# Kernel optimization log

Measured on AMD Instinct MI355X. Metric: run time of the kernel, lower is better.

Reference implementation:

```python
import jax, jax.numpy as jnp
import numpy as np

B, S, H, E, K = 4, 4096, 2048, 64, 2
LN_EPS = 1e-5
AUX_EPS = 1e-9


def setup_inputs() -> dict:
    key = jax.random.key(0)
    ks = jax.random.split(key, 5)
    lim1 = 1.0 / np.sqrt(H)
    x = jax.random.normal(ks[0], (B, S, H), dtype=jnp.float32)
    W1 = jax.random.uniform(ks[1], (H, H), jnp.float32, -lim1, lim1)
    b1 = jax.random.uniform(ks[2], (H,), jnp.float32, -lim1, lim1)
    W2 = jax.random.uniform(ks[3], (H, E), jnp.float32, -lim1, lim1)
    b2 = jax.random.uniform(ks[4], (E,), jnp.float32, -lim1, lim1)
    gamma = jnp.ones((H,), jnp.float32)
    beta = jnp.zeros((H,), jnp.float32)
    return {"x": x, "W1": W1, "b1": b1, "W2": W2, "b2": b2, "gamma": gamma, "beta": beta}


def reference(x, W1, b1, W2, b2, gamma, beta):
    # LayerNorm over hidden dim
    mu = jnp.mean(x, axis=-1, keepdims=True)
    var = jnp.mean(jnp.square(x - mu), axis=-1, keepdims=True)
    x_norm = (x - mu) * jax.lax.rsqrt(var + LN_EPS) * gamma + beta
    # 2-layer router MLP: Linear -> ReLU -> Linear
    h = jax.nn.relu(jnp.einsum('bsh,hk->bsk', x_norm, W1) + b1)
    logits = jnp.einsum('bsh,he->bse', h, W2) + b2  # [B,S,E]
    probs = jax.nn.softmax(logits, axis=-1)
    # top-k + renormalize
    top_k_probs, top_k_indices = jax.lax.top_k(probs, K)
    top_k_probs = top_k_probs / jnp.sum(top_k_probs, axis=-1, keepdims=True)
    # aux load-balancing loss
    p_expert = jnp.mean(probs, axis=(0, 1))  # [E]
    aux_loss = jnp.sum(p_expert * jnp.log(p_expert * E + AUX_EPS))
    return top_k_indices, top_k_probs, aux_loss
```

## Files before the change

### kernel.cpp

```cpp
#include <hip/hip_runtime.h>
#include <hip/hip_fp16.h>
#include <cstdint>
#include <cstddef>

#define HH   2048
#define MM   16384
#define NE   64
#define FIXCAP 3072
#define MARGIN 1.0e-3f
#define LN_EPS  1e-5f
#define AUX_EPS 1e-9f

typedef __attribute__((ext_vector_type(8))) _Float16 f16x8;
typedef __attribute__((ext_vector_type(4))) _Float16 f16x4;
typedef __attribute__((ext_vector_type(4))) float    f32x4;

__device__ __forceinline__ void gload_lds16(const void* g, void* l) {
    __builtin_amdgcn_global_load_lds(
        (const __attribute__((address_space(1))) unsigned int*)g,
        (__attribute__((address_space(3))) unsigned int*)l,
        16, 0, 0);
}

__device__ __forceinline__ uint32_t swz64(uint32_t x) {
    return x ^ (((x >> 7) & 3u) << 4) ^ (((x >> 9) & 1u) << 6);
}
__device__ __forceinline__ uint32_t swz128(uint32_t x) {
    return x ^ (((x >> 8) & 7u) << 4);
}

__global__ __launch_bounds__(256) void k_tw1(const float* __restrict__ W1,
                                             _Float16* __restrict__ whp,
                                             _Float16* __restrict__ wlp) {
    __shared__ float tile[32][33];
    int tx = threadIdx.x & 31;
    int ty = threadIdx.x >> 5;
    int bx = blockIdx.x & 63;
    int by = blockIdx.x >> 6;
#pragma unroll
    for (int i = 0; i < 4; ++i) {
        int k = by * 32 + ty + i * 8;
        tile[ty + i * 8][tx] = W1[(size_t)k * HH + bx * 32 + tx];
    }
    __syncthreads();
#pragma unroll
    for (int i = 0; i < 4; ++i) {
        int n = bx * 32 + ty + i * 8;
        float w = tile[tx][ty + i * 8];
        _Float16 hi = (_Float16)w;
        _Float16 lo = (_Float16)((w - (float)hi) * 1024.0f);
        whp[(size_t)n * HH + by * 32 + tx] = hi;
        wlp[(size_t)n * HH + by * 32 + tx] = lo;
    }
}

__global__ __launch_bounds__(256) void k_w2q(const float* __restrict__ W2,
                                             _Float16* __restrict__ w2q) {
    int e = blockIdx.x;
    int t = threadIdx.x;
#pragma unroll
    for (int j = 0; j < 8; ++j) {
        int c = t * 8 + j;
        float w = W2[(size_t)c * NE + e];
        _Float16 hi = (_Float16)w;
        _Float16 lo = (_Float16)((w - (float)hi) * 1024.0f);
        f16x4 q = {hi, hi, lo, (_Float16)0.0f};
        *(f16x4*)&w2q[(size_t)e * 8192 + (size_t)c * 4] = q;
    }
}

__global__ __launch_bounds__(256) void k_ln(const float* __restrict__ x,
                                            const float* __restrict__ gamma,
                                            const float* __restrict__ beta,
                                            _Float16* __restrict__ xh,
                                            _Float16* __restrict__ xl) {
    int row = blockIdx.x * 4 + (threadIdx.x >> 6);
    int lane = threadIdx.x & 63;
    const float4* xr = (const float4*)(x + (size_t)row * HH);
    float4 v[8];
    float s = 0.f, sq = 0.f;
#pragma unroll
    for (int j = 0; j < 8; ++j) {
        v[j] = xr[lane + j * 64];
        s  += v[j].x + v[j].y + v[j].z + v[j].w;
        sq += v[j].x*v[j].x + v[j].y*v[j].y + v[j].z*v[j].z + v[j].w*v[j].w;
    }
#pragma unroll
    for (int m = 1; m < 64; m <<= 1) { s += __shfl_xor(s, m); sq += __shfl_xor(sq, m); }
    float mu  = s * (1.0f / HH);
    float var = sq * (1.0f / HH) - mu * mu;
    float rr  = rsqrtf(var + LN_EPS);

    const float4* gr = (const float4*)gamma;
    const float4* br = (const float4*)beta;
#pragma unroll
    for (int j = 0; j < 8; ++j) {
        int idx = lane + j * 64;
        float4 g = gr[idx];
        float4 b = br[idx];
        float f[4];
        f[0] = (v[j].x - mu) * rr * g.x + b.x;
        f[1] = (v[j].y - mu) * rr * g.y + b.y;
        f[2] = (v[j].z - mu) * rr * g.z + b.z;
        f[3] = (v[j].w - mu) * rr * g.w + b.w;
        f16x4 oh, ol;
#pragma unroll
        for (int q = 0; q < 4; ++q) {
            _Float16 hi = (_Float16)f[q];
            oh[q] = hi;
            ol[q] = (_Float16)(f[q] - (float)hi);
        }
        *(f16x4*)&xh[(size_t)row * HH + idx * 4] = oh;
        *(f16x4*)&xl[(size_t)row * HH + idx * 4] = ol;
    }
}

#define VMW(N) do { asm volatile("s_waitcnt vmcnt(" #N ")" ::: "memory"); \
                    __builtin_amdgcn_sched_barrier(0); } while (0)

#define STAGE1(KT) do { uint32_t kb = (uint32_t)(KT) * 64;                     \
    char* dst = lds + (((KT) & 3) << 15);                                      \
    gload_lds16(pxh + gA0 + kb, dst + dstb0);                                  \
    gload_lds16(pxh + gA1 + kb, dst + dstb1);                                  \
    gload_lds16(pwh + gB0 + kb, dst + 16384 + dstb0);                          \
    gload_lds16(pwh + gB1 + kb, dst + 16384 + dstb1);                          \
} while (0)

__global__ __launch_bounds__(512, 2) void k_gemm1(const _Float16* __restrict__ Ah_g,
                                                  const _Float16* __restrict__ Bh_g,
                                                  const _Float16* __restrict__ w2q,
                                                  const float* __restrict__ b1,
                                                  float* __restrict__ part) {
    __shared__ __align__(16) char lds[131072];

    int xcd = blockIdx.x & 7;
    int idx = blockIdx.x >> 3;
    int bm  = xcd * 8 + (idx >> 3);
    int bn  = idx & 7;
    int t = threadIdx.x;
    int lane = t & 63;
    int wid = t >> 6;
    int wm = wid >> 2;
    int wn = wid & 3;
    int r16 = lane & 15, ko = lane >> 4;

    f32x4 acc[8][4];
#pragma unroll
    for (int m = 0; m < 8; ++m)
#pragma unroll
        for (int n = 0; n < 4; ++n)
            acc[m][n] = (f32x4){0.f, 0.f, 0.f, 0.f};

    const char* pxh = (const char*)Ah_g;
    const char* pwh = (const char*)Bh_g;

    uint32_t dstb0 = (uint32_t)t * 16;
    uint32_t dstb1 = 8192 + dstb0;
    uint32_t L0 = swz64(dstb0), L1 = swz64(dstb1);
    uint32_t gA0 = ((uint32_t)bm * 256 + (L0 >> 6)) * (HH * 2) + (L0 & 63);
    uint32_t gA1 = ((uint32_t)bm * 256 + (L1 >> 6)) * (HH * 2) + (L1 & 63);
    uint32_t gB0 = ((uint32_t)bn * 256 + (L0 >> 6)) * (HH * 2) + (L0 & 63);
    uint32_t gB1 = ((uint32_t)bn * 256 + (L1 >> 6)) * (HH * 2) + (L1 & 63);

    uint32_t aoff[8], boff[4];
#pragma unroll
    for (int m = 0; m < 8; ++m)
        aoff[m] = swz64((uint32_t)(wm * 128 + m * 16 + r16) * 64 + ko * 16);
#pragma unroll
    for (int n = 0; n < 4; ++n)
        boff[n] = swz64((uint32_t)(wn * 64 + n * 16 + r16) * 64 + ko * 16);

    STAGE1(0);
    STAGE1(1);
    STAGE1(2);
    VMW(8);
    __builtin_amdgcn_s_barrier();

    for (int kt = 0; kt < 64; ++kt) {
        char* slot = lds + ((kt & 3) << 15);
        const char* Axh = slot;
        const char* Bwh = slot + 16384;

        f16x8 fbh[4], fah[4];
#pragma unroll
        for (int n = 0; n < 4; ++n) fbh[n] = *(const f16x8*)(Bwh + boff[n]);
#pragma unroll
        for (int m = 0; m < 4; ++m) fah[m] = *(const f16x8*)(Axh + aoff[m]);
        if (kt < 61) STAGE1(kt + 3);
        __builtin_amdgcn_s_setprio(1);
#pragma unroll
        for (int m = 0; m < 4; ++m)
#pragma unroll
            for (int n = 0; n < 4; ++n)
                acc[m][n] = __builtin_amdgcn_mfma_f32_16x16x32_f16(fah[m], fbh[n], acc[m][n], 0, 0, 0);
        __builtin_amdgcn_s_setprio(0);
#pragma unroll
        for (int m = 0; m < 4; ++m) fah[m] = *(const f16x8*)(Axh + aoff[4 + m]);
        __builtin_amdgcn_s_setprio(1);
#pragma unroll
        for (int m = 0; m < 4; ++m)
#pragma unroll
            for (int n = 0; n < 4; ++n)
                acc[4 + m][n] = __builtin_amdgcn_mfma_f32_16x16x32_f16(fah[m], fbh[n], acc[4 + m][n], 0, 0, 0);
        __builtin_amdgcn_s_setprio(0);
        if (kt < 61)      VMW(8);
        else if (kt == 61) VMW(4);
        else if (kt == 62) VMW(0);
        __builtin_amdgcn_s_barrier();
    }

    char* A2 = lds;
    char* B2 = lds + 32768;

    float bv[4];
#pragma unroll
    for (int n = 0; n < 4; ++n)
        bv[n] = b1[bn * 256 + wn * 64 + n * 16 + r16];

    f32x4 acc2[2][4];
#pragma unroll
    for (int mf = 0; mf < 2; ++mf)
#pragma unroll
        for (int ef = 0; ef < 4; ++ef)
            acc2[mf][ef] = (f32x4){0.f, 0.f, 0.f, 0.f};

    int hi4 = lane >> 4;
    int ko16 = ko * 16;

#pragma unroll
    for (int c = 0; c < 16; ++c) {
        {
            int e = t >> 3;
            int cb = (t & 7) * 16;
            const char* src = (const char*)w2q + (size_t)e * 16384
                            + (size_t)bn * 2048 + (size_t)c * 128 + cb;
            *(f16x8*)(B2 + swz128((uint32_t)e * 128 + cb)) = *(const f16x8*)src;
        }
        if (wn == (c >> 2)) {
            const int n = c & 3;
#pragma unroll
            for (int m = 0; m < 8; ++m)
#pragma unroll
                for (int i = 0; i < 4; ++i) {
                    float h = acc[m][n][i] + bv[n];
                    h = fmaxf(h, 0.f);
                    _Float16 hh = (_Float16)h;
                    float hhf = (float)hh;
                    _Float16 hl = (_Float16)(h - hhf);
                    _Float16 hs = (_Float16)(hhf * 0.0009765625f);
                    int row = wm * 128 + m * 16 + hi4 * 4 + i;
                    f16x4 q = {hh, hl, hs, (_Float16)0.0f};
                    *(f16x4*)(A2 + swz128((uint32_t)row * 128 + r16 * 8)) = q;
                }
        }
        __syncthreads();
#pragma unroll
        for (int kk = 0; kk < 2; ++kk) {
            f16x8 bfr[4];
#pragma unroll
            for (int ef = 0; ef < 4; ++ef)
                bfr[ef] = *(const f16x8*)(B2 +
                    swz128((uint32_t)(ef * 16 + r16) * 128 + kk * 64 + ko16));
#pragma unroll
            for (int mf = 0; mf < 2; ++mf) {
                f16x8 afr = *(const f16x8*)(A2 +
                    swz128((uint32_t)(wid * 32 + mf * 16 + r16) * 128 + kk * 64 + ko16));
#pragma unroll
                for (int ef = 0; ef < 4; ++ef)
                    acc2[mf][ef] = __builtin_amdgcn_mfma_f32_16x16x32_f16(
                        afr, bfr[ef], acc2[mf][ef], 0, 0, 0);
            }
        }
        __syncthreads();
    }

#pragma unroll
    for (int mf = 0; mf < 2; ++mf)
#pragma unroll
        for (int i = 0; i < 4; ++i) {
            int grow = bm * 256 + wid * 32 + mf * 16 + hi4 * 4 + i;
            float* dst = part + ((size_t)bn * MM + grow) * NE;
#pragma unroll
            for (int ef = 0; ef < 4; ++ef)
                dst[ef * 16 + r16] = acc2[mf][ef][i];
        }
}

__global__ __launch_bounds__(64) void k_screen(const float* __restrict__ part,
                                               const float* __restrict__ b2,
                                               float* __restrict__ out,
                                               float* __restrict__ sums,
                                               int* __restrict__ list,
                                               int* __restrict__ cnt) {
    int lane = threadIdx.x;
    int r = blockIdx.x * 64 + lane;
    float l[NE];
#pragma unroll
    for (int e = 0; e < NE; e += 4) {
        float4 b = *(const float4*)&b2[e];
        l[e] = b.x; l[e + 1] = b.y; l[e + 2] = b.z; l[e + 3] = b.w;
    }
    for (int sl = 0; sl < 8; ++sl) {
        const float* ps = part + ((size_t)sl * MM + r) * NE;
#pragma unroll
        for (int e = 0; e < NE; e += 4) {
            float4 v = *(const float4*)&ps[e];
            l[e] += v.x; l[e + 1] += v.y; l[e + 2] += v.z; l[e + 3] += v.w;
        }
    }
    float m1 = -1e30f, m2 = -1e30f, m3 = -1e30f;
    int i1 = 0, i2 = 0;
#pragma unroll
    for (int e = 0; e < NE; ++e) {
        if (l[e] > m1)      { m3 = m2; m2 = m1; i2 = i1; m1 = l[e]; i1 = e; }
        else if (l[e] > m2) { m3 = m2; m2 = l[e]; i2 = e; }
        else if (l[e] > m3) { m3 = l[e]; }
    }
    float ev[NE];
    float Z = 0.f;
#pragma unroll
    for (int e = 0; e < NE; ++e) { ev[e] = expf(l[e] - m1); Z += ev[e]; }

    float eb = expf(m2 - m1);
    float pa = 1.0f / (1.0f + eb);
    float pb = eb * pa;

    out[(size_t)r * 2 + 0] = (float)i1;
    out[(size_t)r * 2 + 1] = (float)i2;
    out[(size_t)2 * MM + r * 2 + 0] = pa;
    out[(size_t)2 * MM + r * 2 + 1] = pb;

    if ((m1 - m2 < MARGIN) || (m2 - m3 < MARGIN)) {
        int s = atomicAdd(cnt, 1);
        if (s < FIXCAP) list[s] = r;
    }

    float invZ = 1.0f / Z;
    float keep = 0.f;
#pragma unroll
    for (int e = 0; e < NE; ++e) {
        float q = ev[e] * invZ;
#pragma unroll
        for (int sh = 1; sh < 64; sh <<= 1) q += __shfl_xor(q, sh);
        if (lane == e) keep = q;
    }
    atomicAdd(&sums[lane], keep);
}

#define VMW0 do { asm volatile("s_waitcnt vmcnt(0)" ::: "memory"); \
                  __builtin_amdgcn_sched_barrier(0); } while (0)

#define STAGEF_A(KT) do { uint32_t kb = (uint32_t)(KT) * 64;                   \
    char* dst = lds + (((KT) & 1) << 16);                                      \
    gload_lds16(pxh + gA0 + kb, dst + dstb0);                                  \
    gload_lds16(pxh + gA1 + kb, dst + dstb1);                                  \
    gload_lds16(pxl + gA0 + kb, dst + 16384 + dstb0);                          \
    gload_lds16(pxl + gA1 + kb, dst + 16384 + dstb1);                          \
} while (0)

#define STAGEF_B(KT) do { uint32_t kb = (uint32_t)(KT) * 64;                   \
    char* dst = lds + (((KT) & 1) << 16) + 32768;                              \
    gload_lds16(pwh + gB0 + kb, dst + dstb0);                                  \
    gload_lds16(pwh + gB1 + kb, dst + dstb1);                                  \
    gload_lds16(pwl + gB0 + kb, dst + 16384 + dstb0);                          \
    gload_lds16(pwl + gB1 + kb, dst + 16384 + dstb1);                          \
} while (0)

__global__ __launch_bounds__(512, 2) void k_fixg(const _Float16* __restrict__ Ah_g,
                                                 const _Float16* __restrict__ Al_g,
                                                 const _Float16* __restrict__ Bh_g,
                                                 const _Float16* __restrict__ Bl_g,
                                                 const int* __restrict__ list,
                                                 const int* __restrict__ cnt,
                                                 float* __restrict__ hpart) {
    int ks = blockIdx.x & 3;
    int bn = (blockIdx.x >> 2) & 7;
    int bm = blockIdx.x >> 5;
    int cv = *cnt; if (cv > FIXCAP) cv = FIXCAP;
    if (bm * 256 >= cv) return;

    __shared__ __align__(16) char lds[131072];
    int t = threadIdx.x;
    int lane = t & 63;
    int wid = t >> 6;
    int wm = wid >> 2;
    int wn = wid & 3;
    int r16 = lane & 15, ko = lane >> 4;

    f32x4 acc[8][4];
#pragma unroll
    for (int m = 0; m < 8; ++m)
#pragma unroll
        for (int n = 0; n < 4; ++n)
            acc[m][n] = (f32x4){0.f, 0.f, 0.f, 0.f};

    const char* pxh = (const char*)Ah_g;
    const char* pxl = (const char*)Al_g;
    const char* pwh = (const char*)Bh_g;
    const char* pwl = (const char*)Bl_g;

    uint32_t dstb0 = (uint32_t)t * 16;
    uint32_t dstb1 = 8192 + dstb0;
    uint32_t L0 = swz64(dstb0), L1 = swz64(dstb1);
    int rA0 = list[bm * 256 + (L0 >> 6)];
    int rA1 = list[bm * 256 + (L1 >> 6)];
    uint32_t kso = (uint32_t)ks * 1024;
    uint32_t gA0 = (uint32_t)rA0 * (HH * 2) + (L0 & 63) + kso;
    uint32_t gA1 = (uint32_t)rA1 * (HH * 2) + (L1 & 63) + kso;
    uint32_t gB0 = ((uint32_t)bn * 256 + (L0 >> 6)) * (HH * 2) + (L0 & 63) + kso;
    uint32_t gB1 = ((uint32_t)bn * 256 + (L1 >> 6)) * (HH * 2) + (L1 & 63) + kso;

    uint32_t aoff[8], boff[4];
#pragma unroll
    for (int m = 0; m < 8; ++m)
        aoff[m] = swz64((uint32_t)(wm * 128 + m * 16 + r16) * 64 + ko * 16);
#pragma unroll
    for (int n = 0; n < 4; ++n)
        boff[n] = swz64((uint32_t)(wn * 64 + n * 16 + r16) * 64 + ko * 16);

    STAGEF_A(0);
    STAGEF_B(0);
    VMW0;
    __builtin_amdgcn_s_barrier();

    for (int kt = 0; kt < 16; ++kt) {
        char* slot = lds + ((kt & 1) << 16);
        const char* Axh = slot;
        const char* Axl = slot + 16384;
        const char* Bwh = slot + 32768;
        const char* Bwl = slot + 49152;

        f16x8 fbh[4], fbl[4], fah[4], fal[4];
#pragma unroll
        for (int n = 0; n < 4; ++n) {
            fbh[n] = *(const f16x8*)(Bwh + boff[n]);
            fbl[n] = *(const f16x8*)(Bwl + boff[n]);
        }
#pragma unroll
        for (int m = 0; m < 4; ++m) {
            fah[m] = *(const f16x8*)(Axh + aoff[m]);
            fal[m] = *(const f16x8*)(Axl + aoff[m]);
        }
        if (kt < 15) STAGEF_A(kt + 1);
        __builtin_amdgcn_s_setprio(1);
#pragma unroll
        for (int m = 0; m < 4; ++m) {
            f16x8 fas = fah[m] * (_Float16)0.0009765625f;
#pragma unroll
            for (int n = 0; n < 4; ++n) {
                acc[m][n] = __builtin_amdgcn_mfma_f32_16x16x32_f16(fah[m], fbh[n], acc[m][n], 0, 0, 0);
                acc[m][n] = __builtin_amdgcn_mfma_f32_16x16x32_f16(fal[m], fbh[n], acc[m][n], 0, 0, 0);
                acc[m][n] = __builtin_amdgcn_mfma_f32_16x16x32_f16(fas,    fbl[n], acc[m][n], 0, 0, 0);
            }
        }
        __builtin_amdgcn_s_setprio(0);

#pragma unroll
        for (int m = 0; m < 4; ++m) {
            fah[m] = *(const f16x8*)(Axh + aoff[4 + m]);
            fal[m] = *(const f16x8*)(Axl + aoff[4 + m]);
        }
        if (kt < 15) STAGEF_B(kt + 1);
        __builtin_amdgcn_s_setprio(1);
#pragma unroll
        for (int m = 0; m < 4; ++m) {
            f16x8 fas = fah[m] * (_Float16)0.0009765625f;
#pragma unroll
            for (int n = 0; n < 4; ++n) {
                acc[4 + m][n] = __builtin_amdgcn_mfma_f32_16x16x32_f16(fah[m], fbh[n], acc[4 + m][n], 0, 0, 0);
                acc[4 + m][n] = __builtin_amdgcn_mfma_f32_16x16x32_f16(fal[m], fbh[n], acc[4 + m][n], 0, 0, 0);
                acc[4 + m][n] = __builtin_amdgcn_mfma_f32_16x16x32_f16(fas,    fbl[n], acc[4 + m][n], 0, 0, 0);
            }
        }
        __builtin_amdgcn_s_setprio(0);
        if (kt < 15) VMW0;
        __builtin_amdgcn_s_barrier();
    }

    float* hp = hpart + (size_t)ks * FIXCAP * HH;
    int hi4 = lane >> 4;
#pragma unroll
    for (int m = 0; m < 8; ++m)
#pragma unroll
        for (int n = 0; n < 4; ++n)
#pragma unroll
            for (int i = 0; i < 4; ++i) {
                int row_l = bm * 256 + wm * 128 + m * 16 + hi4 * 4 + i;
                int col = bn * 256 + wn * 64 + n * 16 + r16;
                hp[(size_t)row_l * HH + col] = acc[m][n][i];
            }
}

__global__ __launch_bounds__(256) void k_fix2(const float* __restrict__ hpart,
                                              const float* __restrict__ b1,
                                              const float* __restrict__ W2,
                                              const float* __restrict__ b2,
                                              const int* __restrict__ list,
                                              const int* __restrict__ cnt,
                                              float* __restrict__ out) {
    int n = *cnt; if (n > FIXCAP) n = FIXCAP;
    int gi = blockIdx.x;
    if (gi >= n) return;
    int r = list[gi];
    int e = threadIdx.x & 63;
    int kg = threadIdx.x >> 6;
    const float* h0 = hpart + (size_t)gi * HH;
    const float* h1 = h0 + (size_t)FIXCAP * HH;
    const float* h2 = h1 + (size_t)FIXCAP * HH;
    const float* h3 = h2 + (size_t)FIXCAP * HH;
    float p = 0.f;
    int k0 = kg * 512;
    for (int k = k0; k < k0 + 512; ++k) {
        float h = ((h0[k] + h1[k]) + (h2[k] + h3[k])) + b1[k];
        h = fmaxf(h, 0.f);
        p = fmaf(h, W2[(size_t)k * NE + e], p);
    }
    __shared__ float red[4][NE];
    red[kg][e] = p;
    __syncthreads();
    if (threadIdx.x < 64) {
        float l = ((red[0][e] + red[1][e]) + (red[2][e] + red[3][e])) + b2[e];
        float m1 = l;
#pragma unroll
        for (int sh = 1; sh < 64; sh <<= 1) m1 = fmaxf(m1, __shfl_xor(m1, sh));
        unsigned long long bb = __ballot(l == m1);
        int i1 = (int)(__ffsll((long long)bb) - 1);
        float l2 = (e == i1) ? -1e30f : l;
        float m2 = l2;
#pragma unroll
        for (int sh = 1; sh < 64; sh <<= 1) m2 = fmaxf(m2, __shfl_xor(m2, sh));
        unsigned long long bb2 = __ballot(l2 == m2);
        int i2 = (int)(__ffsll((long long)bb2) - 1);
        if (e == 0) {
            float eb = expf(m2 - m1);
            float pa = 1.0f / (1.0f + eb);
            float pb = eb * pa;
            out[(size_t)r * 2 + 0] = (float)i1;
            out[(size_t)r * 2 + 1] = (float)i2;
            out[(size_t)2 * MM + r * 2 + 0] = pa;
            out[(size_t)2 * MM + r * 2 + 1] = pb;
        }
    }
}

__global__ void k_aux(const float* __restrict__ sums, float* __restrict__ out) {
    if (threadIdx.x == 0) {
        float loss = 0.f;
        for (int e = 0; e < NE; ++e) {
            float p = sums[e] * (1.0f / MM);
            loss += p * logf(p * (float)NE + AUX_EPS);
        }
        out[(size_t)4 * MM] = loss;
    }
}

extern "C" void kernel_launch(void* const* d_in, const int* in_sizes, int n_in,
                              void* d_out, int out_size, void* d_ws, size_t ws_size,
                              hipStream_t stream) {
    const float* x     = (const float*)d_in[0];
    const float* W1    = (const float*)d_in[1];
    const float* b1    = (const float*)d_in[2];
    const float* W2    = (const float*)d_in[3];
    const float* b2    = (const float*)d_in[4];
    const float* gamma = (const float*)d_in[5];
    const float* beta  = (const float*)d_in[6];
    float* out = (float*)d_out;

    char* ws = (char*)d_ws;
    _Float16* xh   = (_Float16*)(ws);
    _Float16* xl   = (_Float16*)(ws + 67108864);
    _Float16* whp  = (_Float16*)(ws + 134217728);
    _Float16* wlp  = (_Float16*)(ws + 142606336);
    _Float16* w2q  = (_Float16*)(ws + 150994944);
    float*    part = (float*)   (ws + 152043520);
    float*   hpart = (float*)   (ws + 152043520);
    int*      list = (int*)     (ws + 252706816);
    float*    sums = (float*)   (ws + 252719104);
    int*      cnt  = (int*)     (ws + 252719360);

    hipMemsetAsync(sums, 0, 512, stream);
    hipMemsetAsync(list, 0, FIXCAP * 4, stream);
    k_tw1   <<<4096,    256, 0, stream>>>(W1, whp, wlp);
    k_w2q   <<<64,      256, 0, stream>>>(W2, w2q);
    k_ln    <<<MM/4,    256, 0, stream>>>(x, gamma, beta, xh, xl);
    k_gemm1 <<<512,     512, 0, stream>>>(xh, whp, w2q, b1, part);
    k_screen<<<MM/64,   64,  0, stream>>>(part, b2, out, sums, list, cnt);
    k_fixg  <<<384,     512, 0, stream>>>(xh, xl, whp, wlp, list, cnt, hpart);
    k_fix2  <<<FIXCAP,  256, 0, stream>>>(hpart, b1, W2, b2, list, cnt, out);
    k_aux   <<<1,       64,  0, stream>>>(sums, out);
}
```

Measured before the change: 368.5 us.

## Compute low-half LN residual only for flagged rows and fuse small kernels

The full LayerNorm pass now writes only the fp16 high part, which removes the 64 MB xl write. A new kernel recomputes LayerNorm hi/lo for just the flagged rows into compact gathered buffers. k_fixg then reads those contiguously instead of gathering through the list. The W1/W2 prep kernels are merged into one launch, the aux-loss kernel is folded into k_fix2, and the two memsets become one, cutting launch count.

```diff
diff --git a/kernel.cpp b/kernel.cpp
--- a/kernel.cpp
+++ b/kernel.cpp
@@ -29,9 +29,25 @@
     return x ^ (((x >> 8) & 7u) << 4);
 }
 
-__global__ __launch_bounds__(256) void k_tw1(const float* __restrict__ W1,
-                                             _Float16* __restrict__ whp,
-                                             _Float16* __restrict__ wlp) {
+__global__ __launch_bounds__(256) void k_prep(const float* __restrict__ W1,
+                                              const float* __restrict__ W2,
+                                              _Float16* __restrict__ whp,
+                                              _Float16* __restrict__ wlp,
+                                              _Float16* __restrict__ w2q) {
+    if (blockIdx.x >= 4096) {
+        int e = blockIdx.x - 4096;
+        int t = threadIdx.x;
+#pragma unroll
+        for (int j = 0; j < 8; ++j) {
+            int c = t * 8 + j;
+            float w = W2[(size_t)c * NE + e];
+            _Float16 hi = (_Float16)w;
+            _Float16 lo = (_Float16)((w - (float)hi) * 1024.0f);
+            f16x4 q = {hi, hi, lo, (_Float16)0.0f};
+            *(f16x4*)&w2q[(size_t)e * 8192 + (size_t)c * 4] = q;
+        }
+        return;
+    }
     __shared__ float tile[32][33];
     int tx = threadIdx.x & 31;
     int ty = threadIdx.x >> 5;
@@ -54,26 +70,10 @@
     }
 }
 
-__global__ __launch_bounds__(256) void k_w2q(const float* __restrict__ W2,
-                                             _Float16* __restrict__ w2q) {
-    int e = blockIdx.x;
-    int t = threadIdx.x;
-#pragma unroll
-    for (int j = 0; j < 8; ++j) {
-        int c = t * 8 + j;
-        float w = W2[(size_t)c * NE + e];
-        _Float16 hi = (_Float16)w;
-        _Float16 lo = (_Float16)((w - (float)hi) * 1024.0f);
-        f16x4 q = {hi, hi, lo, (_Float16)0.0f};
-        *(f16x4*)&w2q[(size_t)e * 8192 + (size_t)c * 4] = q;
-    }
-}
-
 __global__ __launch_bounds__(256) void k_ln(const float* __restrict__ x,
                                             const float* __restrict__ gamma,
                                             const float* __restrict__ beta,
-                                            _Float16* __restrict__ xh,
-                                            _Float16* __restrict__ xl) {
+                                            _Float16* __restrict__ xh) {
     int row = blockIdx.x * 4 + (threadIdx.x >> 6);
     int lane = threadIdx.x & 63;
     const float4* xr = (const float4*)(x + (size_t)row * HH);
@@ -98,20 +98,12 @@
         int idx = lane + j * 64;
         float4 g = gr[idx];
         float4 b = br[idx];
-        float f[4];
-        f[0] = (v[j].x - mu) * rr * g.x + b.x;
-        f[1] = (v[j].y - mu) * rr * g.y + b.y;
-        f[2] = (v[j].z - mu) * rr * g.z + b.z;
-        f[3] = (v[j].w - mu) * rr * g.w + b.w;
-        f16x4 oh, ol;
-#pragma unroll
-        for (int q = 0; q < 4; ++q) {
-            _Float16 hi = (_Float16)f[q];
-            oh[q] = hi;
-            ol[q] = (_Float16)(f[q] - (float)hi);
-        }
+        f16x4 oh;
+        oh[0] = (_Float16)((v[j].x - mu) * rr * g.x + b.x);
+        oh[1] = (_Float16)((v[j].y - mu) * rr * g.y + b.y);
+        oh[2] = (_Float16)((v[j].z - mu) * rr * g.z + b.z);
+        oh[3] = (_Float16)((v[j].w - mu) * rr * g.w + b.w);
         *(f16x4*)&xh[(size_t)row * HH + idx * 4] = oh;
-        *(f16x4*)&xl[(size_t)row * HH + idx * 4] = ol;
     }
 }
 
@@ -347,6 +339,61 @@
     atomicAdd(&sums[lane], keep);
 }
 
+__global__ __launch_bounds__(256) void k_lnx(const float* __restrict__ x,
+                                             const float* __restrict__ gamma,
+                                             const float* __restrict__ beta,
+                                             const int* __restrict__ list,
+                                             const int* __restrict__ cnt,
+                                             _Float16* __restrict__ xhg,
+                                             _Float16* __restrict__ xlg) {
+    int n = *cnt; if (n > FIXCAP) n = FIXCAP;
+    int gi = blockIdx.x;
+    if (gi >= n) return;
+    int row = list[gi];
+    int t = threadIdx.x;
+    const float4* xr = (const float4*)(x + (size_t)row * HH);
+    float4 v0 = xr[t];
+    float4 v1 = xr[t + 256];
+    float s  = v0.x + v0.y + v0.z + v0.w + v1.x + v1.y + v1.z + v1.w;
+    float sq = v0.x*v0.x + v0.y*v0.y + v0.z*v0.z + v0.w*v0.w
+             + v1.x*v1.x + v1.y*v1.y + v1.z*v1.z + v1.w*v1.w;
+#pragma unroll
+    for (int m = 1; m < 64; m <<= 1) { s += __shfl_xor(s, m); sq += __shfl_xor(sq, m); }
+    __shared__ float red[8];
+    int wv = t >> 6;
+    if ((t & 63) == 0) { red[wv] = s; red[wv + 4] = sq; }
+    __syncthreads();
+    s  = red[0] + red[1] + red[2] + red[3];
+    sq = red[4] + red[5] + red[6] + red[7];
+    float mu  = s * (1.0f / HH);
+    float var = sq * (1.0f / HH) - mu * mu;
+    float rr  = rsqrtf(var + LN_EPS);
+
+    const float4* gr = (const float4*)gamma;
+    const float4* br = (const float4*)beta;
+#pragma unroll
+    for (int p = 0; p < 2; ++p) {
+        int idx = t + p * 256;
+        float4 v = (p == 0) ? v0 : v1;
+        float4 g = gr[idx];
+        float4 b = br[idx];
+        float f[4];
+        f[0] = (v.x - mu) * rr * g.x + b.x;
+        f[1] = (v.y - mu) * rr * g.y + b.y;
+        f[2] = (v.z - mu) * rr * g.z + b.z;
+        f[3] = (v.w - mu) * rr * g.w + b.w;
+        f16x4 oh, ol;
+#pragma unroll
+        for (int j = 0; j < 4; ++j) {
+            _Float16 hi = (_Float16)f[j];
+            oh[j] = hi;
+            ol[j] = (_Float16)(f[j] - (float)hi);
+        }
+        *(f16x4*)&xhg[(size_t)gi * HH + idx * 4] = oh;
+        *(f16x4*)&xlg[(size_t)gi * HH + idx * 4] = ol;
+    }
+}
+
 #define VMW0 do { asm volatile("s_waitcnt vmcnt(0)" ::: "memory"); \
                   __builtin_amdgcn_sched_barrier(0); } while (0)
 
@@ -370,7 +417,6 @@
                                                  const _Float16* __restrict__ Al_g,
                                                  const _Float16* __restrict__ Bh_g,
                                                  const _Float16* __restrict__ Bl_g,
-                                                 const int* __restrict__ list,
                                                  const int* __restrict__ cnt,
                                                  float* __restrict__ hpart) {
     int ks = blockIdx.x & 3;
@@ -402,11 +448,9 @@
     uint32_t dstb0 = (uint32_t)t * 16;
     uint32_t dstb1 = 8192 + dstb0;
     uint32_t L0 = swz64(dstb0), L1 = swz64(dstb1);
-    int rA0 = list[bm * 256 + (L0 >> 6)];
-    int rA1 = list[bm * 256 + (L1 >> 6)];
     uint32_t kso = (uint32_t)ks * 1024;
-    uint32_t gA0 = (uint32_t)rA0 * (HH * 2) + (L0 & 63) + kso;
-    uint32_t gA1 = (uint32_t)rA1 * (HH * 2) + (L1 & 63) + kso;
+    uint32_t gA0 = ((uint32_t)bm * 256 + (L0 >> 6)) * (HH * 2) + (L0 & 63) + kso;
+    uint32_t gA1 = ((uint32_t)bm * 256 + (L1 >> 6)) * (HH * 2) + (L1 & 63) + kso;
     uint32_t gB0 = ((uint32_t)bn * 256 + (L0 >> 6)) * (HH * 2) + (L0 & 63) + kso;
     uint32_t gB1 = ((uint32_t)bn * 256 + (L1 >> 6)) * (HH * 2) + (L1 & 63) + kso;
 
@@ -497,7 +541,16 @@
                                               const float* __restrict__ b2,
                                               const int* __restrict__ list,
                                               const int* __restrict__ cnt,
+                                              const float* __restrict__ sums,
                                               float* __restrict__ out) {
+    if (blockIdx.x == 0 && threadIdx.x == 0) {
+        float loss = 0.f;
+        for (int e = 0; e < NE; ++e) {
+            float p = sums[e] * (1.0f / MM);
+            loss += p * logf(p * (float)NE + AUX_EPS);
+        }
+        out[(size_t)4 * MM] = loss;
+    }
     int n = *cnt; if (n > FIXCAP) n = FIXCAP;
     int gi = blockIdx.x;
     if (gi >= n) return;
@@ -543,17 +596,6 @@
     }
 }
 
-__global__ void k_aux(const float* __restrict__ sums, float* __restrict__ out) {
-    if (threadIdx.x == 0) {
-        float loss = 0.f;
-        for (int e = 0; e < NE; ++e) {
-            float p = sums[e] * (1.0f / MM);
-            loss += p * logf(p * (float)NE + AUX_EPS);
-        }
-        out[(size_t)4 * MM] = loss;
-    }
-}
-
 extern "C" void kernel_launch(void* const* d_in, const int* in_sizes, int n_in,
                               void* d_out, int out_size, void* d_ws, size_t ws_size,
                               hipStream_t stream) {
@@ -568,24 +610,23 @@
 
     char* ws = (char*)d_ws;
     _Float16* xh   = (_Float16*)(ws);
-    _Float16* xl   = (_Float16*)(ws + 67108864);
-    _Float16* whp  = (_Float16*)(ws + 134217728);
-    _Float16* wlp  = (_Float16*)(ws + 142606336);
-    _Float16* w2q  = (_Float16*)(ws + 150994944);
-    float*    part = (float*)   (ws + 152043520);
-    float*   hpart = (float*)   (ws + 152043520);
-    int*      list = (int*)     (ws + 252706816);
-    float*    sums = (float*)   (ws + 252719104);
-    int*      cnt  = (int*)     (ws + 252719360);
-
-    hipMemsetAsync(sums, 0, 512, stream);
-    hipMemsetAsync(list, 0, FIXCAP * 4, stream);
-    k_tw1   <<<4096,    256, 0, stream>>>(W1, whp, wlp);
-    k_w2q   <<<64,      256, 0, stream>>>(W2, w2q);
-    k_ln    <<<MM/4,    256, 0, stream>>>(x, gamma, beta, xh, xl);
+    _Float16* whp  = (_Float16*)(ws + 67108864);
+    _Float16* wlp  = (_Float16*)(ws + 75497472);
+    _Float16* w2q  = (_Float16*)(ws + 83886080);
+    float*    part = (float*)   (ws + 84934656);
+    float*   hpart = (float*)   (ws + 84934656);
+    _Float16* xhg  = (_Float16*)(ws + 185597952);
+    _Float16* xlg  = (_Float16*)(ws + 198180864);
+    int*      list = (int*)     (ws + 210763776);
+    float*    sums = (float*)   (ws + 210776064);
+    int*      cnt  = (int*)     (ws + 210776320);
+
+    hipMemsetAsync(list, 0, 12548, stream);
+    k_prep  <<<4160,    256, 0, stream>>>(W1, W2, whp, wlp, w2q);
+    k_ln    <<<MM/4,    256, 0, stream>>>(x, gamma, beta, xh);
     k_gemm1 <<<512,     512, 0, stream>>>(xh, whp, w2q, b1, part);
     k_screen<<<MM/64,   64,  0, stream>>>(part, b2, out, sums, list, cnt);
-    k_fixg  <<<384,     512, 0, stream>>>(xh, xl, whp, wlp, list, cnt, hpart);
-    k_fix2  <<<FIXCAP,  256, 0, stream>>>(hpart, b1, W2, b2, list, cnt, out);
-    k_aux   <<<1,       64,  0, stream>>>(sums, out);
-}
+    k_lnx   <<<FIXCAP,  256, 0, stream>>>(x, gamma, beta, list, cnt, xhg, xlg);
+    k_fixg  <<<384,     512, 0, stream>>>(xhg, xlg, whp, wlp, cnt, hpart);
+    k_fix2  <<<FIXCAP,  256, 0, stream>>>(hpart, b1, W2, b2, list, cnt, sums, out);
+}
```

New measurement: 339.9 us (median of 2 runs). 7.8% less time.
